# Kernel tuning notes

Measured on AMD Instinct MI355X. Metric: run time of the kernel, lower is better.

The kernel has to match this reference:

```python
import jax, jax.numpy as jnp
import numpy as np
from jax import lax

B, V, M, C, CM, D = 48, 16, 32, 48, 8, 128
VOCAB_V, VOCAB_M, OUT = 2000, 1000, 256


def setup_inputs() -> dict:
    key = jax.random.key(0)
    ks = jax.random.split(key, 22)
    s = 0.1  # keep GRU gates out of saturation
    return {
        "visit_ids": jax.random.randint(ks[0], (3, B, V, C), 0, VOCAB_V),
        "mon_ids": jax.random.randint(ks[1], (4, B, V, M, CM), 0, VOCAB_M),
        "weight_vals": jax.random.uniform(ks[2], (B, V)),
        "age_vals": jax.random.uniform(ks[3], (B, V)),
        "emb_visit": jax.random.normal(ks[4], (3, VOCAB_V, D)) * s,
        "emb_mon": jax.random.normal(ks[5], (4, VOCAB_M, D)) * s,
        "mgru_Wih": jax.random.normal(ks[6], (5, 3 * D, D)) * s,
        "mgru_Whh": jax.random.normal(ks[7], (5, 3 * D, D)) * s,
        "mgru_bih": jax.random.normal(ks[8], (5, 3 * D)) * s,
        "mgru_bhh": jax.random.normal(ks[9], (5, 3 * D)) * s,
        "vgru_Wih": jax.random.normal(ks[10], (7, 3 * D, D)) * s,
        "vgru_Whh": jax.random.normal(ks[11], (7, 3 * D, D)) * s,
        "vgru_bih": jax.random.normal(ks[12], (7, 3 * D)) * s,
        "vgru_bhh": jax.random.normal(ks[13], (7, 3 * D)) * s,
        "fc_weight_w": jax.random.normal(ks[14], (D, 1)) * s,
        "fc_weight_b": jax.random.normal(ks[15], (D,)) * s,
        "fc_age_w": jax.random.normal(ks[16], (D, 1)) * s,
        "fc_age_b": jax.random.normal(ks[17], (D,)) * s,
        "fc_out_w": jax.random.normal(ks[18], (OUT, 7 * D)) * s,
        "fc_out_b": jax.random.normal(ks[19], (OUT,)) * s,
    }


def gru_last(x, Wih, Whh, bih, bhh):
    """torch.nn.GRU(batch_first=True), return final hidden [N, D]."""
    xi = jnp.einsum('ntd,ed->nte', x, Wih) + bih  # [N, T, 3D] input projections
    h0 = jnp.zeros((x.shape[0], Whh.shape[1]), x.dtype)

    def step(h, gi):
        gh = h @ Whh.T + bhh
        ir, iz, inn = jnp.split(gi, 3, axis=-1)
        hr, hz, hn = jnp.split(gh, 3, axis=-1)
        r = jax.nn.sigmoid(ir + hr)
        z = jax.nn.sigmoid(iz + hz)
        n = jnp.tanh(inn + r * hn)
        return (1.0 - z) * n + z * h, None

    hT, _ = lax.scan(step, h0, jnp.swapaxes(xi, 0, 1))
    return hT


def reference(visit_ids, mon_ids, weight_vals, age_vals, emb_visit, emb_mon,
              mgru_Wih, mgru_Whh, mgru_bih, mgru_bhh,
              vgru_Wih, vgru_Whh, vgru_bih, vgru_bhh,
              fc_weight_w, fc_weight_b, fc_age_w, fc_age_b,
              fc_out_w, fc_out_b):
    # padding_idx=0 -> zero embedding row (dropout in eval mode = identity)
    ev = emb_visit.at[:, 0].set(0.0)
    em = emb_mon.at[:, 0].set(0.0)

    # visit-event embedding-bag: sum over code dim -> [B, V, D] per feature
    visit_origin = [jnp.sum(ev[k][visit_ids[k]], axis=2) for k in range(3)]

    def run_stream(t, mi, vi):
        # monitor-level GRU over M, then visit-level GRU over V
        h1 = gru_last(t, mgru_Wih[mi], mgru_Whh[mi], mgru_bih[mi], mgru_bhh[mi])
        h2 = gru_last(h1.reshape(B, V, D),
                      vgru_Wih[vi], vgru_Whh[vi], vgru_bih[vi], vgru_bhh[vi])
        return h2  # [B, D]

    # output slots in dict-insertion order: lab_item, cond, proc, drug, inj_item, weight, age
    slots = [None] * 7
    for p in range(2):  # (lab_item, lab_value), (inj_item, inj_value)
        # elementwise item*value embedding, summed over codes -> [B*V, M, D]
        mon = jnp.sum(em[2 * p][mon_ids[2 * p]] * em[2 * p + 1][mon_ids[2 * p + 1]],
                      axis=3).reshape(B * V, M, D)
        slots[0 if p == 0 else 4] = run_stream(mon, p, p)
        for k in range(3):  # visit features repeated along monitor dim
            t = jnp.broadcast_to(visit_origin[k][:, :, None, :],
                                 (B, V, M, D)).reshape(B * V, M, D)
            h = run_stream(t, 2 + k, 2 + k)
            slots[1 + k] = h if slots[1 + k] is None else slots[1 + k] + h

    # weight / age: Linear(1->D), zero-mask, visit-level GRU
    for vals, w, b, vi, slot in ((weight_vals, fc_weight_w, fc_weight_b, 5, 5),
                                 (age_vals, fc_age_w, fc_age_b, 6, 6)):
        xf = vals.reshape(-1, 1)
        h = (xf @ w.T + b) * (xf != 0)
        slots[slot] = gru_last(h.reshape(B, V, D),
                               vgru_Wih[vi], vgru_Whh[vi], vgru_bih[vi], vgru_bhh[vi])

    patient_emb = jnp.concatenate(slots, axis=-1)  # [B, 7D]
    return jax.nn.relu(patient_emb) @ fc_out_w.T + fc_out_b
```

## Files before the change

kernel.cpp:

```cpp
#include <hip/hip_runtime.h>
#include <stdint.h>


typedef unsigned short u16;
typedef uint32_t u32;
typedef short bf8 __attribute__((ext_vector_type(8)));
typedef float f4 __attribute__((ext_vector_type(4)));

static __device__ __forceinline__ float bf2f(u16 b){ u32 u=((u32)b)<<16; float f; __builtin_memcpy(&f,&u,4); return f; }
static __device__ __forceinline__ u16 f2bf(float f){ u32 u; __builtin_memcpy(&u,&f,4); u32 r=(u+0x7fffu+((u>>16)&1u))>>16; return (u16)r; }
static __device__ __forceinline__ float bflo(u32 u){ u32 x=u<<16; float f; __builtin_memcpy(&f,&x,4); return f; }
static __device__ __forceinline__ float bfhi(u32 u){ u32 x=u&0xffff0000u; float f; __builtin_memcpy(&f,&x,4); return f; }
static __device__ __forceinline__ f4 mfma16(bf8 a, bf8 b, f4 c){ return __builtin_amdgcn_mfma_f32_16x16x32_bf16(a,b,c,0,0,0); }

#if __has_builtin(__builtin_amdgcn_exp2f)
static __device__ __forceinline__ float fexp2(float x){ return __builtin_amdgcn_exp2f(x); }
#else
static __device__ __forceinline__ float fexp2(float x){ float r; asm volatile("v_exp_f32 %0, %1" : "=v"(r) : "v"(x)); return r; }
#endif
#if __has_builtin(__builtin_amdgcn_rcpf)
static __device__ __forceinline__ float frcp(float x){ return __builtin_amdgcn_rcpf(x); }
#else
static __device__ __forceinline__ float frcp(float x){ float r; asm volatile("v_rcp_f32 %0, %1" : "=v"(r) : "v"(x)); return r; }
#endif
#define LOG2E 1.44269504089f
static __device__ __forceinline__ float sigm(float x){ return frcp(1.0f + fexp2(-LOG2E*x)); }
static __device__ __forceinline__ float tanh_f(float x){ return 1.0f - 2.0f*frcp(1.0f + fexp2((2.0f*LOG2E)*x)); }

__global__ __launch_bounds__(256) void k_prep(
    const float* __restrict__ s0, const float* __restrict__ s1,
    const float* __restrict__ s2, const float* __restrict__ s3,
    const float* __restrict__ s4, const float* __restrict__ s5,
    u16* __restrict__ d0, u16* __restrict__ d1, u16* __restrict__ d2,
    u16* __restrict__ d3, u16* __restrict__ d4, u16* __restrict__ d5){
  int i = blockIdx.x*256 + threadIdx.x;
  const float* s; u16* d; int off;
  if      (i < 61440)  { s=s0; d=d0; off=i; }
  else if (i < 122880) { s=s1; d=d1; off=i-61440; }
  else if (i < 208896) { s=s2; d=d2; off=i-122880; }
  else if (i < 294912) { s=s3; d=d3; off=i-208896; }
  else if (i < 422912) { s=s4; d=d4; off=i-294912; }
  else if (i < 614912) { s=s5; d=d5; off=i-422912; }
  else return;
  float4 v = *(const float4*)(s + (size_t)off*4);
  ushort4 o = { f2bf(v.x), f2bf(v.y), f2bf(v.z), f2bf(v.w) };
  *(ushort4*)(d + (size_t)off*4) = o;
}

__global__ __launch_bounds__(256) void k_bags(const int* __restrict__ vids, const int* __restrict__ mids,
    const u16* __restrict__ embv_b, const u16* __restrict__ embm_b,
    const float* __restrict__ wv, const float* __restrict__ av,
    const float* __restrict__ ww, const float* __restrict__ wb,
    const float* __restrict__ aw, const float* __restrict__ ab,
    u16* __restrict__ mon_xT, u16* __restrict__ vis_org, u16* __restrict__ hin2T){
  int y = blockIdx.y;
  if (y < 2){
    int p = y;
    int rid = threadIdx.x >> 5, lane32 = threadIdx.x & 31, d0 = lane32*4;
    __shared__ int ids[8][16];
    if (threadIdx.x < 128){
      int rr = threadIdx.x >> 4, c = threadIdx.x & 15;
      int f = 2*p + (c>>3), cm = c & 7;
      ids[rr][c] = mids[((size_t)f*24576 + (size_t)blockIdx.x*8 + rr)*8 + cm];
    }
    __syncthreads();
    const u16* e1 = embm_b + (size_t)(2*p)*1000*128;
    const u16* e2 = embm_b + (size_t)(2*p+1)*1000*128;
    float a0=0.f,a1=0.f,a2=0.f,a3=0.f;
    #pragma unroll
    for (int c = 0; c < 8; ++c){
      int i1 = ids[rid][c], i2 = ids[rid][8+c];
      if (i1 && i2){
        uint2 a = *(const uint2*)(e1 + (size_t)i1*128 + d0);
        uint2 b = *(const uint2*)(e2 + (size_t)i2*128 + d0);
        a0 += bflo(a.x)*bflo(b.x); a1 += bfhi(a.x)*bfhi(b.x);
        a2 += bflo(a.y)*bflo(b.y); a3 += bfhi(a.y)*bfhi(b.y);
      }
    }
    size_t nm = (size_t)blockIdx.x*8 + rid;
    int bv = (int)(nm >> 5), m = (int)(nm & 31);
    ushort4 o = { f2bf(a0), f2bf(a1), f2bf(a2), f2bf(a3) };
    *(ushort4*)(mon_xT + (size_t)p*24576*128 + ((size_t)m*768 + bv)*128 + d0) = o;
  } else {
    int x = blockIdx.x;
    int sub = threadIdx.x >> 7, d = threadIdx.x & 127;
    if (x < 1152){
      __shared__ int ids[2][48];
      int row = x*2 + sub;
      int k = row / 768, bv = row - k*768;
      if (d < 48) ids[sub][d] = vids[((size_t)k*768 + bv)*48 + d];
      __syncthreads();
      const u16* eb = embv_b + (size_t)k*2000*128;
      float acc = 0.f;
      #pragma unroll 4
      for (int c = 0; c < 48; ++c){ int id = ids[sub][c]; if (id) acc += bf2f(eb[(size_t)id*128 + d]); }
      vis_org[((size_t)k*768 + bv)*128 + d] = f2bf(acc);
    } else if (x < 1920){
      int grow = (x - 1152)*2 + sub;
      int sidx = grow >= 768 ? 1 : 0;
      int row = grow - sidx*768;
      const float* vals = sidx ? av : wv;
      const float* wgt  = sidx ? aw : ww;
      const float* bias = sidx ? ab : wb;
      float v = vals[row];
      float h = (v != 0.f) ? (v * wgt[d] + bias[d]) : 0.f;
      int b = row >> 4, vv = row & 15;
      hin2T[((size_t)(5+sidx)*768 + (size_t)vv*48 + b)*128 + d] = f2bf(h);
    }
  }
}


#define BARRIER() asm volatile("s_waitcnt lgkmcnt(0)\n\ts_barrier" ::: "memory")

#define ALOAD(S, tt) { int t_=(tt); if (t_>=T) t_=0; \
  const u16* p_ = ap + (size_t)t_*rstride; \
  S[0]=*(const bf8*)(p_); S[1]=*(const bf8*)(p_+32); \
  S[2]=*(const bf8*)(p_+64); S[3]=*(const bf8*)(p_+96); }

#define GIMM(G0,G1,G2,S) { \
  f4 t0_={bs0_,bs0_,bs0_,bs0_}; G0=t0_; \
  f4 t1_={bs1_,bs1_,bs1_,bs1_}; G1=t1_; \
  f4 t2_={bin_,bin_,bin_,bin_}; G2=t2_; \
  G0=mfma16(S[0],wfi[0][0],G0); G0=mfma16(S[1],wfi[0][1],G0); \
  G0=mfma16(S[2],wfi[0][2],G0); G0=mfma16(S[3],wfi[0][3],G0); \
  G1=mfma16(S[0],wfi[1][0],G1); G1=mfma16(S[1],wfi[1][1],G1); \
  G1=mfma16(S[2],wfi[1][2],G1); G1=mfma16(S[3],wfi[1][3],G1); \
  G2=mfma16(S[0],wfi[2][0],G2); G2=mfma16(S[1],wfi[2][1],G2); \
  G2=mfma16(S[2],wfi[2][2],G2); G2=mfma16(S[3],wfi[2][3],G2); }

#define GH(G0,G1,AN) { \
  bf8 hf0_=*(const bf8*)&hlds[cur][lr][lq*8]; \
  bf8 hf1_=*(const bf8*)&hlds[cur][lr][32+lq*8]; \
  bf8 hf2_=*(const bf8*)&hlds[cur][lr][64+lq*8]; \
  bf8 hf3_=*(const bf8*)&hlds[cur][lr][96+lq*8]; \
  f4 an_={bhn_,bhn_,bhn_,bhn_}; AN=an_; \
  G0=mfma16(hf0_,wfh[0][0],G0); G0=mfma16(hf1_,wfh[0][1],G0); \
  G0=mfma16(hf2_,wfh[0][2],G0); G0=mfma16(hf3_,wfh[0][3],G0); \
  G1=mfma16(hf0_,wfh[1][0],G1); G1=mfma16(hf1_,wfh[1][1],G1); \
  G1=mfma16(hf2_,wfh[1][2],G1); G1=mfma16(hf3_,wfh[1][3],G1); \
  AN=mfma16(hf0_,wfh[2][0],AN); AN=mfma16(hf1_,wfh[2][1],AN); \
  AN=mfma16(hf2_,wfh[2][2],AN); AN=mfma16(hf3_,wfh[2][3],AN); }

#define GATES(G0,G1,G2,AN) { int nxt_=cur^1; \
  _Pragma("unroll") \
  for (int r=0;r<4;++r){ \
    float rr_=sigm(G0[r]); \
    float zz_=sigm(G1[r]); \
    float nn_=tanh_f(G2[r]+rr_*AN[r]); \
    float hv_=(1.0f-zz_)*nn_+zz_*hp[r]; hp[r]=hv_; \
    hlds[nxt_][lq*4+r][w*16+lr]=f2bf(hv_); } \
  BARRIER(); cur=nxt_; }

#define STEPB(G0,G1,G2,SN,tt) { \
  GH(G0,G1,ANr); \
  GATES(G0,G1,G2,ANr); \
  if ((tt)+2 < T){ GIMM(G0,G1,G2,SN); } \
  ALOAD(SN,(tt)+4); }

__global__ __launch_bounds__(512, 2) void k_gru(int phase,
    const u16* __restrict__ mon_xT, const u16* __restrict__ vis_org,
    u16* __restrict__ hin2T, u16* __restrict__ h2,
    const u16* __restrict__ mWih, const float* __restrict__ mbih,
    const u16* __restrict__ mWhh, const float* __restrict__ mbhh,
    const u16* __restrict__ vWih, const float* __restrict__ vbih,
    const u16* __restrict__ vWhh, const float* __restrict__ vbhh){
  int s = blockIdx.y, g = blockIdx.x;
  const u16* A; size_t rstride; int T, oMode; u16* ho;
  const u16 *Wi, *Wh; const float *biP, *bhP;
  if (phase == 0 && s < 5){
    T = 32; oMode = 0;
    if (s < 2){ A = mon_xT + (size_t)s*24576*128; rstride = 768*128; }
    else      { A = vis_org + (size_t)(s-2)*768*128; rstride = 0; }
    Wi = mWih + (size_t)s*49152; Wh = mWhh + (size_t)s*49152;
    biP = mbih + (size_t)s*384;  bhP = mbhh + (size_t)s*384;
    int slot = (0x32140u >> (4*s)) & 15;
    ho = hin2T + (size_t)slot*768*128;
  } else {
    if (g >= 3) return;
    T = 16; oMode = 1;
    A = hin2T + (size_t)s*768*128; rstride = 48*128;
    int vi = (0x6514320u >> (4*s)) & 15;
    Wi = vWih + (size_t)vi*49152; Wh = vWhh + (size_t)vi*49152;
    biP = vbih + (size_t)vi*384;  bhP = vbhh + (size_t)vi*384;
    ho = h2 + (size_t)s*48*128;
  }

  int w = threadIdx.x >> 6, l = threadIdx.x & 63;
  int lr = l & 15, lq = l >> 4;

  bf8 wfi[3][4], wfh[3][4];
  #pragma unroll
  for (int j = 0; j < 3; ++j){
    int colb = (w + 8*j)*16;
    const u16* wpi = Wi + (size_t)(colb + lr)*128 + lq*8;
    const u16* wph = Wh + (size_t)(colb + lr)*128 + lq*8;
    #pragma unroll
    for (int kt = 0; kt < 4; ++kt){
      wfi[j][kt] = *(const bf8*)(wpi + kt*32);
      wfh[j][kt] = *(const bf8*)(wph + kt*32);
    }
  }
  float bs0_ = biP[w*16 + lr]      + bhP[w*16 + lr];
  float bs1_ = biP[(8+w)*16 + lr]  + bhP[(8+w)*16 + lr];
  float bin_ = biP[(16+w)*16 + lr];
  float bhn_ = bhP[(16+w)*16 + lr];

  const u16* ap = A + (size_t)(g*16 + lr)*128 + lq*8;
  __shared__ u16 hlds[2][16][132];
  float hp[4] = {0.f,0.f,0.f,0.f};
  int cur = 0;
  f4 ANr;

  if (rstride){
    bf8 S0[4], S1[4];
    f4 gE0,gE1,gE2, gO0,gO1,gO2;
    ALOAD(S0,0); ALOAD(S1,1);
    GIMM(gE0,gE1,gE2,S0); ALOAD(S0,2);
    GIMM(gO0,gO1,gO2,S1); ALOAD(S1,3);
    {
      f4 an0={bhn_,bhn_,bhn_,bhn_}; ANr=an0;
      GATES(gE0,gE1,gE2,ANr);
    }
    GIMM(gE0,gE1,gE2,S0); ALOAD(S0,4);
    STEPB(gO0,gO1,gO2,S1,1);
    for (int t = 2; t < T; t += 2){
      STEPB(gE0,gE1,gE2,S0,t);
      STEPB(gO0,gO1,gO2,S1,t+1);
    }
  } else {
    f4 C0,C1,C2;
    {
      bf8 S0[4];
      ALOAD(S0,0);
      GIMM(C0,C1,C2,S0);
    }
    {
      f4 an0={bhn_,bhn_,bhn_,bhn_}; ANr=an0;
      GATES(C0,C1,C2,ANr);
    }
    for (int t = 1; t < T; ++t){
      f4 G0=C0, G1=C1;
      GH(G0,G1,ANr);
      GATES(G0,G1,C2,ANr);
    }
  }

  if (oMode == 0){
    #pragma unroll
    for (int r = 0; r < 4; ++r)
      ho[((size_t)(lq*4+r)*48 + g)*128 + w*16 + lr] = f2bf(hp[r]);
  } else {
    #pragma unroll
    for (int r = 0; r < 4; ++r)
      ho[((size_t)(g*16 + lq*4 + r))*128 + w*16 + lr] = f2bf(hp[r]);
  }
}

__global__ __launch_bounds__(256) void k_final(const u16* __restrict__ h2,
                                               const float* __restrict__ W,
                                               const float* __restrict__ Bias,
                                               float* __restrict__ out){
  int b = blockIdx.x, t = threadIdx.x;
  __shared__ float emb[896];
  for (int i = t; i < 896; i += 256){
    int j = i >> 7, d = i & 127;
    float v = bf2f(h2[((size_t)j*48 + b)*128 + d]);
    if (j >= 1 && j <= 3) v *= 2.0f;
    emb[i] = fmaxf(v, 0.f);
  }
  __syncthreads();
  float acc = Bias[t];
  const float* wp = W + (size_t)t*896;
  for (int i = 0; i < 896; i += 8){
    float4 w0 = *(const float4*)(wp + i);
    float4 w1 = *(const float4*)(wp + i + 4);
    acc += w0.x*emb[i]   + w0.y*emb[i+1] + w0.z*emb[i+2] + w0.w*emb[i+3];
    acc += w1.x*emb[i+4] + w1.y*emb[i+5] + w1.z*emb[i+6] + w1.w*emb[i+7];
  }
  out[(size_t)b*256 + t] = acc;
}

extern "C" void kernel_launch(void* const* d_in, const int* in_sizes, int n_in,
                              void* d_out, int out_size, void* d_ws, size_t ws_size,
                              hipStream_t stream){
  const int*   visit_ids   = (const int*)d_in[0];
  const int*   mon_ids     = (const int*)d_in[1];
  const float* weight_vals = (const float*)d_in[2];
  const float* age_vals    = (const float*)d_in[3];
  const float* emb_visit   = (const float*)d_in[4];
  const float* emb_mon     = (const float*)d_in[5];
  const float* mgru_Wih    = (const float*)d_in[6];
  const float* mgru_Whh    = (const float*)d_in[7];
  const float* mgru_bih    = (const float*)d_in[8];
  const float* mgru_bhh    = (const float*)d_in[9];
  const float* vgru_Wih    = (const float*)d_in[10];
  const float* vgru_Whh    = (const float*)d_in[11];
  const float* vgru_bih    = (const float*)d_in[12];
  const float* vgru_bhh    = (const float*)d_in[13];
  const float* fc_w_w      = (const float*)d_in[14];
  const float* fc_w_b      = (const float*)d_in[15];
  const float* fc_a_w      = (const float*)d_in[16];
  const float* fc_a_b      = (const float*)d_in[17];
  const float* fc_out_w    = (const float*)d_in[18];
  const float* fc_out_b    = (const float*)d_in[19];

  char* ws = (char*)d_ws;
  size_t o = 0;
  u16* mWih_b  = (u16*)(ws+o); o += 5ull*384*128*2;
  u16* mWhh_b  = (u16*)(ws+o); o += 5ull*384*128*2;
  u16* vWih_b  = (u16*)(ws+o); o += 7ull*384*128*2;
  u16* vWhh_b  = (u16*)(ws+o); o += 7ull*384*128*2;
  u16* embm_b  = (u16*)(ws+o); o += 4ull*1000*128*2;
  u16* embv_b  = (u16*)(ws+o); o += 3ull*2000*128*2;
  u16* mon_xT  = (u16*)(ws+o); o += 2ull*24576*128*2;
  u16* vis_org = (u16*)(ws+o); o += 3ull*768*128*2;
  u16* hin2T   = (u16*)(ws+o); o += 7ull*768*128*2;
  u16* h2      = (u16*)(ws+o); o += 7ull*48*128*2;

  k_prep<<<2402, 256, 0, stream>>>(mgru_Wih, mgru_Whh, vgru_Wih, vgru_Whh, emb_mon, emb_visit,
                                   mWih_b, mWhh_b, vWih_b, vWhh_b, embm_b, embv_b);
  k_bags<<<dim3(3072,3), 256, 0, stream>>>(visit_ids, mon_ids, embv_b, embm_b,
      weight_vals, age_vals, fc_w_w, fc_w_b, fc_a_w, fc_a_b,
      mon_xT, vis_org, hin2T);
  k_gru<<<dim3(48,7), 512, 0, stream>>>(0, mon_xT, vis_org, hin2T, h2,
      mWih_b, mgru_bih, mWhh_b, mgru_bhh, vWih_b, vgru_bih, vWhh_b, vgru_bhh);
  k_gru<<<dim3(3,5), 512, 0, stream>>>(1, mon_xT, vis_org, hin2T, h2,
      mWih_b, mgru_bih, mWhh_b, mgru_bhh, vWih_b, vgru_bih, vWhh_b, vgru_bhh);
  k_final<<<48, 256, 0, stream>>>(h2, fc_out_w, fc_out_b, (float*)d_out);
}
```

Measured before the change: 140.4 us.

## Fold activation scale constants into GRU weights and widen embedding-bag loads

GRU weights and biases are pre-scaled by -log2(e) for the r/z gates and 2·log2(e) for the n gate during bf16 conversion. This removes the per-element multiply inside sigmoid/tanh on the recurrent critical path, and the hidden update is rewritten as nn + z*(h - nn). The embedding-bag kernel now handles more rows per block with 16-byte loads, and the visit bag uses vectorized 4-wide lanes instead of scalar per-dim loads. The GRU launch grids are trimmed so no blocks early-exit. Scaling the weights before bf16 rounding slightly changes numerics.

```diff
diff --git a/kernel.cpp b/kernel.cpp
--- a/kernel.cpp
+++ b/kernel.cpp
@@ -24,8 +24,7 @@
 static __device__ __forceinline__ float frcp(float x){ float r; asm volatile("v_rcp_f32 %0, %1" : "=v"(r) : "v"(x)); return r; }
 #endif
 #define LOG2E 1.44269504089f
-static __device__ __forceinline__ float sigm(float x){ return frcp(1.0f + fexp2(-LOG2E*x)); }
-static __device__ __forceinline__ float tanh_f(float x){ return 1.0f - 2.0f*frcp(1.0f + fexp2((2.0f*LOG2E)*x)); }
+#define TWOL  2.88539008178f
 
 __global__ __launch_bounds__(256) void k_prep(
     const float* __restrict__ s0, const float* __restrict__ s1,
@@ -34,16 +33,18 @@
     u16* __restrict__ d0, u16* __restrict__ d1, u16* __restrict__ d2,
     u16* __restrict__ d3, u16* __restrict__ d4, u16* __restrict__ d5){
   int i = blockIdx.x*256 + threadIdx.x;
-  const float* s; u16* d; int off;
+  const float* s; u16* d; int off; bool scaled = true;
   if      (i < 61440)  { s=s0; d=d0; off=i; }
   else if (i < 122880) { s=s1; d=d1; off=i-61440; }
   else if (i < 208896) { s=s2; d=d2; off=i-122880; }
   else if (i < 294912) { s=s3; d=d3; off=i-208896; }
-  else if (i < 422912) { s=s4; d=d4; off=i-294912; }
-  else if (i < 614912) { s=s5; d=d5; off=i-422912; }
+  else if (i < 422912) { s=s4; d=d4; off=i-294912; scaled=false; }
+  else if (i < 614912) { s=s5; d=d5; off=i-422912; scaled=false; }
   else return;
+  float sc = 1.0f;
+  if (scaled){ int row = (off >> 5) % 384; sc = (row < 256) ? -LOG2E : TWOL; }
   float4 v = *(const float4*)(s + (size_t)off*4);
-  ushort4 o = { f2bf(v.x), f2bf(v.y), f2bf(v.z), f2bf(v.w) };
+  ushort4 o = { f2bf(v.x*sc), f2bf(v.y*sc), f2bf(v.z*sc), f2bf(v.w*sc) };
   *(ushort4*)(d + (size_t)off*4) = o;
 }
 
@@ -56,56 +57,78 @@
   int y = blockIdx.y;
   if (y < 2){
     int p = y;
-    int rid = threadIdx.x >> 5, lane32 = threadIdx.x & 31, d0 = lane32*4;
-    __shared__ int ids[8][16];
-    if (threadIdx.x < 128){
+    int rid = threadIdx.x >> 4, lane16 = threadIdx.x & 15, dd0 = lane16*8;
+    __shared__ int ids[16][16];
+    {
       int rr = threadIdx.x >> 4, c = threadIdx.x & 15;
-      int f = 2*p + (c>>3), cm = c & 7;
-      ids[rr][c] = mids[((size_t)f*24576 + (size_t)blockIdx.x*8 + rr)*8 + cm];
+      int f = 2*p + (c >> 3), cm = c & 7;
+      ids[rr][c] = mids[((size_t)f*24576 + (size_t)blockIdx.x*16 + rr)*8 + cm];
     }
     __syncthreads();
     const u16* e1 = embm_b + (size_t)(2*p)*1000*128;
     const u16* e2 = embm_b + (size_t)(2*p+1)*1000*128;
-    float a0=0.f,a1=0.f,a2=0.f,a3=0.f;
+    float a0=0.f,a1=0.f,a2=0.f,a3=0.f,a4=0.f,a5=0.f,a6=0.f,a7=0.f;
     #pragma unroll
     for (int c = 0; c < 8; ++c){
       int i1 = ids[rid][c], i2 = ids[rid][8+c];
       if (i1 && i2){
-        uint2 a = *(const uint2*)(e1 + (size_t)i1*128 + d0);
-        uint2 b = *(const uint2*)(e2 + (size_t)i2*128 + d0);
+        uint4 a = *(const uint4*)(e1 + (size_t)i1*128 + dd0);
+        uint4 b = *(const uint4*)(e2 + (size_t)i2*128 + dd0);
         a0 += bflo(a.x)*bflo(b.x); a1 += bfhi(a.x)*bfhi(b.x);
         a2 += bflo(a.y)*bflo(b.y); a3 += bfhi(a.y)*bfhi(b.y);
+        a4 += bflo(a.z)*bflo(b.z); a5 += bfhi(a.z)*bfhi(b.z);
+        a6 += bflo(a.w)*bflo(b.w); a7 += bfhi(a.w)*bfhi(b.w);
       }
     }
-    size_t nm = (size_t)blockIdx.x*8 + rid;
+    size_t nm = (size_t)blockIdx.x*16 + rid;
     int bv = (int)(nm >> 5), m = (int)(nm & 31);
-    ushort4 o = { f2bf(a0), f2bf(a1), f2bf(a2), f2bf(a3) };
-    *(ushort4*)(mon_xT + (size_t)p*24576*128 + ((size_t)m*768 + bv)*128 + d0) = o;
+    uint4 o;
+    o.x = (u32)f2bf(a0) | ((u32)f2bf(a1) << 16);
+    o.y = (u32)f2bf(a2) | ((u32)f2bf(a3) << 16);
+    o.z = (u32)f2bf(a4) | ((u32)f2bf(a5) << 16);
+    o.w = (u32)f2bf(a6) | ((u32)f2bf(a7) << 16);
+    *(uint4*)(mon_xT + (size_t)p*24576*128 + ((size_t)m*768 + bv)*128 + dd0) = o;
   } else {
     int x = blockIdx.x;
-    int sub = threadIdx.x >> 7, d = threadIdx.x & 127;
-    if (x < 1152){
-      __shared__ int ids[2][48];
-      int row = x*2 + sub;
+    if (x < 288){
+      __shared__ int ids[8][48];
+      for (int i = threadIdx.x; i < 384; i += 256){
+        int rr = i / 48, c = i - rr*48;
+        int row = x*8 + rr;
+        int k = row / 768, bv = row - k*768;
+        ids[rr][c] = vids[((size_t)k*768 + bv)*48 + c];
+      }
+      __syncthreads();
+      int rid = threadIdx.x >> 5, lane = threadIdx.x & 31, dd0 = lane*4;
+      int row = x*8 + rid;
       int k = row / 768, bv = row - k*768;
-      if (d < 48) ids[sub][d] = vids[((size_t)k*768 + bv)*48 + d];
-      __syncthreads();
       const u16* eb = embv_b + (size_t)k*2000*128;
-      float acc = 0.f;
+      float a0=0.f,a1=0.f,a2=0.f,a3=0.f;
       #pragma unroll 4
-      for (int c = 0; c < 48; ++c){ int id = ids[sub][c]; if (id) acc += bf2f(eb[(size_t)id*128 + d]); }
-      vis_org[((size_t)k*768 + bv)*128 + d] = f2bf(acc);
-    } else if (x < 1920){
-      int grow = (x - 1152)*2 + sub;
-      int sidx = grow >= 768 ? 1 : 0;
-      int row = grow - sidx*768;
-      const float* vals = sidx ? av : wv;
-      const float* wgt  = sidx ? aw : ww;
-      const float* bias = sidx ? ab : wb;
-      float v = vals[row];
-      float h = (v != 0.f) ? (v * wgt[d] + bias[d]) : 0.f;
-      int b = row >> 4, vv = row & 15;
-      hin2T[((size_t)(5+sidx)*768 + (size_t)vv*48 + b)*128 + d] = f2bf(h);
+      for (int c = 0; c < 48; ++c){
+        int id = ids[rid][c];
+        if (id){
+          uint2 a = *(const uint2*)(eb + (size_t)id*128 + dd0);
+          a0 += bflo(a.x); a1 += bfhi(a.x);
+          a2 += bflo(a.y); a3 += bfhi(a.y);
+        }
+      }
+      ushort4 o = { f2bf(a0), f2bf(a1), f2bf(a2), f2bf(a3) };
+      *(ushort4*)(vis_org + ((size_t)k*768 + bv)*128 + dd0) = o;
+    } else if (x < 672){
+      int sub = threadIdx.x >> 7, d = threadIdx.x & 127;
+      for (int h2i = 0; h2i < 2; ++h2i){
+        int grow = (x - 288)*4 + sub*2 + h2i;
+        int sidx = grow >= 768 ? 1 : 0;
+        int row = grow - sidx*768;
+        const float* vals = sidx ? av : wv;
+        const float* wgt  = sidx ? aw : ww;
+        const float* bias = sidx ? ab : wb;
+        float v = vals[row];
+        float h = (v != 0.f) ? (v * wgt[d] + bias[d]) : 0.f;
+        int b = row >> 4, vv = row & 15;
+        hin2T[((size_t)(5+sidx)*768 + (size_t)vv*48 + b)*128 + d] = f2bf(h);
+      }
     }
   }
 }
@@ -145,10 +168,10 @@
 #define GATES(G0,G1,G2,AN) { int nxt_=cur^1; \
   _Pragma("unroll") \
   for (int r=0;r<4;++r){ \
-    float rr_=sigm(G0[r]); \
-    float zz_=sigm(G1[r]); \
-    float nn_=tanh_f(G2[r]+rr_*AN[r]); \
-    float hv_=(1.0f-zz_)*nn_+zz_*hp[r]; hp[r]=hv_; \
+    float rr_=frcp(1.0f+fexp2(G0[r])); \
+    float zz_=frcp(1.0f+fexp2(G1[r])); \
+    float nn_=1.0f-2.0f*frcp(1.0f+fexp2(G2[r]+rr_*AN[r])); \
+    float hv_=nn_+zz_*(hp[r]-nn_); hp[r]=hv_; \
     hlds[nxt_][lq*4+r][w*16+lr]=f2bf(hv_); } \
   BARRIER(); cur=nxt_; }
 
@@ -168,7 +191,7 @@
   int s = blockIdx.y, g = blockIdx.x;
   const u16* A; size_t rstride; int T, oMode; u16* ho;
   const u16 *Wi, *Wh; const float *biP, *bhP;
-  if (phase == 0 && s < 5){
+  if (phase == 0){
     T = 32; oMode = 0;
     if (s < 2){ A = mon_xT + (size_t)s*24576*128; rstride = 768*128; }
     else      { A = vis_org + (size_t)(s-2)*768*128; rstride = 0; }
@@ -177,7 +200,6 @@
     int slot = (0x32140u >> (4*s)) & 15;
     ho = hin2T + (size_t)slot*768*128;
   } else {
-    if (g >= 3) return;
     T = 16; oMode = 1;
     A = hin2T + (size_t)s*768*128; rstride = 48*128;
     int vi = (0x6514320u >> (4*s)) & 15;
@@ -201,10 +223,10 @@
       wfh[j][kt] = *(const bf8*)(wph + kt*32);
     }
   }
-  float bs0_ = biP[w*16 + lr]      + bhP[w*16 + lr];
-  float bs1_ = biP[(8+w)*16 + lr]  + bhP[(8+w)*16 + lr];
-  float bin_ = biP[(16+w)*16 + lr];
-  float bhn_ = bhP[(16+w)*16 + lr];
+  float bs0_ = -LOG2E*(biP[w*16 + lr]     + bhP[w*16 + lr]);
+  float bs1_ = -LOG2E*(biP[(8+w)*16 + lr] + bhP[(8+w)*16 + lr]);
+  float bin_ =  TWOL*biP[(16+w)*16 + lr];
+  float bhn_ =  TWOL*bhP[(16+w)*16 + lr];
 
   const u16* ap = A + (size_t)(g*16 + lr)*128 + lq*8;
   __shared__ u16 hlds[2][16][132];
@@ -218,10 +240,8 @@
     ALOAD(S0,0); ALOAD(S1,1);
     GIMM(gE0,gE1,gE2,S0); ALOAD(S0,2);
     GIMM(gO0,gO1,gO2,S1); ALOAD(S1,3);
-    {
-      f4 an0={bhn_,bhn_,bhn_,bhn_}; ANr=an0;
-      GATES(gE0,gE1,gE2,ANr);
-    }
+    { f4 an0={bhn_,bhn_,bhn_,bhn_}; ANr=an0;
+      GATES(gE0,gE1,gE2,ANr); }
     GIMM(gE0,gE1,gE2,S0); ALOAD(S0,4);
     STEPB(gO0,gO1,gO2,S1,1);
     for (int t = 2; t < T; t += 2){
@@ -230,15 +250,9 @@
     }
   } else {
     f4 C0,C1,C2;
-    {
-      bf8 S0[4];
-      ALOAD(S0,0);
-      GIMM(C0,C1,C2,S0);
-    }
-    {
-      f4 an0={bhn_,bhn_,bhn_,bhn_}; ANr=an0;
-      GATES(C0,C1,C2,ANr);
-    }
+    { bf8 S0[4]; ALOAD(S0,0); GIMM(C0,C1,C2,S0); }
+    { f4 an0={bhn_,bhn_,bhn_,bhn_}; ANr=an0;
+      GATES(C0,C1,C2,ANr); }
     for (int t = 1; t < T; ++t){
       f4 G0=C0, G1=C1;
       GH(G0,G1,ANr);
@@ -320,12 +334,12 @@
 
   k_prep<<<2402, 256, 0, stream>>>(mgru_Wih, mgru_Whh, vgru_Wih, vgru_Whh, emb_mon, emb_visit,
                                    mWih_b, mWhh_b, vWih_b, vWhh_b, embm_b, embv_b);
-  k_bags<<<dim3(3072,3), 256, 0, stream>>>(visit_ids, mon_ids, embv_b, embm_b,
+  k_bags<<<dim3(1536,3), 256, 0, stream>>>(visit_ids, mon_ids, embv_b, embm_b,
       weight_vals, age_vals, fc_w_w, fc_w_b, fc_a_w, fc_a_b,
       mon_xT, vis_org, hin2T);
-  k_gru<<<dim3(48,7), 512, 0, stream>>>(0, mon_xT, vis_org, hin2T, h2,
+  k_gru<<<dim3(48,5), 512, 0, stream>>>(0, mon_xT, vis_org, hin2T, h2,
       mWih_b, mgru_bih, mWhh_b, mgru_bhh, vWih_b, vgru_bih, vWhh_b, vgru_bhh);
-  k_gru<<<dim3(3,5), 512, 0, stream>>>(1, mon_xT, vis_org, hin2T, h2,
+  k_gru<<<dim3(3,7), 512, 0, stream>>>(1, mon_xT, vis_org, hin2T, h2,
       mWih_b, mgru_bih, mWhh_b, mgru_bhh, vWih_b, vgru_bih, vWhh_b, vgru_bhh);
   k_final<<<48, 256, 0, stream>>>(h2, fc_out_w, fc_out_b, (float*)d_out);
 }
```

After: 122.9 us. 12.4% less time.
